# Optimization experiments

Measured on AMD Instinct MI355X. Metric: run time of the kernel, lower is better.

The kernel has to match this reference:

```python
import jax, jax.numpy as jnp
import numpy as np

N_NODES = 50000
N_EDGES = 800000
N_GRAPHS = 512
IN_CH = 7
HID = 128
FC = 128
N_CLASSES = 2
NEG_SLOPE = 0.2


def setup_inputs() -> dict:
    key = jax.random.key(0)
    ks = jax.random.split(key, 20)
    x = jax.random.normal(ks[0], (N_NODES, IN_CH), dtype=jnp.float32)
    edge_index = jax.random.randint(ks[1], (2, N_EDGES), 0, N_NODES, dtype=jnp.int64)
    batch = jnp.sort(jax.random.randint(ks[2], (N_NODES,), 0, N_GRAPHS, dtype=jnp.int64))
    inp = {"x": x, "edge_index": edge_index, "batch": batch}
    dims = [(IN_CH, HID), (HID, HID), (HID, HID)]
    for l, (din, dout) in enumerate(dims):
        inp[f"W{l}"] = jax.random.normal(ks[3 + 4 * l], (din, dout), dtype=jnp.float32) * (1.0 / np.sqrt(din))
        inp[f"a_src{l}"] = jax.random.normal(ks[4 + 4 * l], (dout,), dtype=jnp.float32) * 0.1
        inp[f"a_dst{l}"] = jax.random.normal(ks[5 + 4 * l], (dout,), dtype=jnp.float32) * 0.1
        inp[f"b{l}"] = jnp.zeros((dout,), dtype=jnp.float32)
    inp["fc1_w"] = jax.random.normal(ks[15], (HID, FC), dtype=jnp.float32) * (1.0 / np.sqrt(HID))
    inp["fc1_b"] = jnp.zeros((FC,), dtype=jnp.float32)
    inp["fc2_w"] = jax.random.normal(ks[16], (FC, N_CLASSES), dtype=jnp.float32) * (1.0 / np.sqrt(FC))
    inp["fc2_b"] = jnp.zeros((N_CLASSES,), dtype=jnp.float32)
    return inp


def _gat_conv(x, src, dst, W, a_s, a_d, b):
    # x: [N, din] -> h: [N, dout]
    h = x @ W
    alpha_src = h @ a_s  # [N]
    alpha_dst = h @ a_d  # [N]
    e = alpha_src[src] + alpha_dst[dst]  # [E]
    e = jnp.where(e > 0, e, NEG_SLOPE * e)  # LeakyReLU(0.2)
    # segment softmax over destination node neighborhoods
    m = jax.ops.segment_max(e, dst, num_segments=N_NODES)
    m = jnp.where(jnp.isfinite(m), m, 0.0)
    e = jnp.exp(e - m[dst])
    s = jax.ops.segment_sum(e, dst, num_segments=N_NODES)
    alpha = e / (s[dst] + 1e-16)  # [E]
    out = jax.ops.segment_sum(alpha[:, None] * h[src], dst, num_segments=N_NODES)
    return out + b


def _forward(x, edge_index, batch, params):
    # PyG GATConv default: add self-loops
    loop = jnp.arange(N_NODES, dtype=edge_index.dtype)
    src = jnp.concatenate([edge_index[0], loop])
    dst = jnp.concatenate([edge_index[1], loop])
    for l in range(3):
        W, a_s, a_d, b = params[f"W{l}"], params[f"a_src{l}"], params[f"a_dst{l}"], params[f"b{l}"]
        x = jax.nn.elu(_gat_conv(x, src, dst, W, a_s, a_d, b))
    # global mean pool over graphs
    sums = jax.ops.segment_sum(x, batch, num_segments=N_GRAPHS)  # [G, HID]
    cnt = jax.ops.segment_sum(jnp.ones((N_NODES,), x.dtype), batch, num_segments=N_GRAPHS)
    g = sums / jnp.maximum(cnt, 1.0)[:, None]
    h = jax.nn.relu(g @ params["fc1_w"] + params["fc1_b"])
    logits = h @ params["fc2_w"] + params["fc2_b"]
    return jax.nn.log_softmax(logits, axis=1)


def reference(x, edge_index, batch, W0, a_src0, a_dst0, b0, W1, a_src1, a_dst1, b1,
              W2, a_src2, a_dst2, b2, fc1_w, fc1_b, fc2_w, fc2_b):
    params = {"W0": W0, "a_src0": a_src0, "a_dst0": a_dst0, "b0": b0,
              "W1": W1, "a_src1": a_src1, "a_dst1": a_dst1, "b1": b1,
              "W2": W2, "a_src2": a_src2, "a_dst2": a_dst2, "b2": b2,
              "fc1_w": fc1_w, "fc1_b": fc1_b, "fc2_w": fc2_w, "fc2_b": fc2_b}
    return _forward(x, edge_index, batch, params)
```

## Files before the change

kernel.cpp:

```cpp
#include <hip/hip_runtime.h>
#include <math.h>

#define N_NODES 50000
#define N_EDGES 800000
#define N_GRAPHS 512
#define IN_CH 7
#define HID 128
#define FC 128
#define ET (N_EDGES + N_NODES)
#define NEG_SLOPE 0.2f


__global__ void k_init_deg(int* __restrict__ deg) {
  int i = blockIdx.x * blockDim.x + threadIdx.x;
  if (i < N_NODES) deg[i] = 1;
}

__global__ void k_hist(const int* __restrict__ dst, int* __restrict__ deg) {
  int i = blockIdx.x * blockDim.x + threadIdx.x;
  if (i < N_EDGES) atomicAdd(&deg[dst[i]], 1);
}

__global__ __launch_bounds__(1024) void k_scan(const int* __restrict__ deg,
                                               int* __restrict__ row_start,
                                               int* __restrict__ cursor) {
  __shared__ int wsum[16];
  __shared__ int s_carry;
  int tid = threadIdx.x;
  int lane = tid & 63, wid = tid >> 6;
  if (tid == 0) s_carry = 0;
  __syncthreads();
  for (int base = 0; base < N_NODES; base += 1024) {
    int i = base + tid;
    int v = (i < N_NODES) ? deg[i] : 0;
    int inc = v;
    #pragma unroll
    for (int off = 1; off < 64; off <<= 1) {
      int t = __shfl_up(inc, off, 64);
      if (lane >= off) inc += t;
    }
    if (lane == 63) wsum[wid] = inc;
    __syncthreads();
    if (wid == 0) {
      int wv = (lane < 16) ? wsum[lane] : 0;
      #pragma unroll
      for (int off = 1; off < 16; off <<= 1) {
        int t = __shfl_up(wv, off, 64);
        if (lane >= off) wv += t;
      }
      if (lane < 16) wsum[lane] = wv;
    }
    __syncthreads();
    int woff = (wid > 0) ? wsum[wid - 1] : 0;
    int incl = s_carry + woff + inc;
    int excl = incl - v;
    if (i < N_NODES) { row_start[i] = excl; cursor[i] = excl; }
    __syncthreads();
    if (tid == 1023) s_carry += wsum[15];
    __syncthreads();
  }
  if (tid == 0) row_start[N_NODES] = s_carry;
}

__global__ void k_fill(const int* __restrict__ esrc, const int* __restrict__ edst,
                       int* __restrict__ cursor, int* __restrict__ csr_src) {
  int i = blockIdx.x * blockDim.x + threadIdx.x;
  if (i < ET) {
    int s, d;
    if (i < N_EDGES) { s = esrc[i]; d = edst[i]; }
    else             { s = d = i - N_EDGES; }
    int pos = atomicAdd(&cursor[d], 1);
    csr_src[pos] = s;
  }
}


template<int DIN, int NPB>
__global__ __launch_bounds__(128) void k_gemm_small(const float* __restrict__ x,
                                                    const float* __restrict__ W,
                                                    const float* __restrict__ a_s,
                                                    const float* __restrict__ a_d,
                                                    float* __restrict__ h,
                                                    float* __restrict__ as_,
                                                    float* __restrict__ ad_) {
  __shared__ float Ws[DIN * HID];
  __shared__ float xs[DIN];
  __shared__ float red[4];
  int tid = threadIdx.x;
  for (int i = tid; i < DIN * HID; i += 128) Ws[i] = W[i];
  float asf = a_s[tid], adf = a_d[tid];
  int node0 = blockIdx.x * NPB;
  for (int nn = 0; nn < NPB; ++nn) {
    int node = node0 + nn;
    if (node >= N_NODES) break;
    __syncthreads();
    if (tid < DIN) xs[tid] = x[(size_t)node * DIN + tid];
    __syncthreads();
    float acc = 0.f;
    #pragma unroll
    for (int k = 0; k < DIN; ++k) acc = fmaf(xs[k], Ws[k * HID + tid], acc);
    h[(size_t)node * HID + tid] = acc;
    float vs = acc * asf, vd = acc * adf;
    #pragma unroll
    for (int off = 32; off >= 1; off >>= 1) {
      vs += __shfl_xor(vs, off, 64);
      vd += __shfl_xor(vd, off, 64);
    }
    int lane = tid & 63, wid = tid >> 6;
    if (lane == 0) { red[wid * 2] = vs; red[wid * 2 + 1] = vd; }
    __syncthreads();
    if (tid == 0)      as_[node] = red[0] + red[2];
    else if (tid == 1) ad_[node] = red[1] + red[3];
  }
}


#define GNPB 32

__global__ __launch_bounds__(128, 2) void k_gemm128(const float* __restrict__ x,
                                                    const float* __restrict__ W,
                                                    const float* __restrict__ a_s,
                                                    const float* __restrict__ a_d,
                                                    float* __restrict__ h,
                                                    float* __restrict__ as_,
                                                    float* __restrict__ ad_) {
  __shared__ float4 xs4[GNPB * 32];
  __shared__ float red[GNPB][4];
  int tid = threadIdx.x;
  int lane = tid & 63, wid = tid >> 6;

  float wreg[HID];
  #pragma unroll
  for (int k = 0; k < HID; ++k) wreg[k] = W[(size_t)k * HID + tid];
  float asf = a_s[tid], adf = a_d[tid];

  int node0 = blockIdx.x * GNPB;
  int rows = N_NODES - node0; if (rows > GNPB) rows = GNPB;

  const float4* xg = (const float4*)(x + (size_t)node0 * HID);
  for (int j = tid; j < rows * 32; j += 128) xs4[j] = xg[j];
  __syncthreads();

  for (int nn = 0; nn < rows; ++nn) {
    float acc = 0.f;
    #pragma unroll
    for (int k4 = 0; k4 < 32; ++k4) {
      float4 xv = xs4[nn * 32 + k4];
      acc = fmaf(xv.x, wreg[4 * k4 + 0], acc);
      acc = fmaf(xv.y, wreg[4 * k4 + 1], acc);
      acc = fmaf(xv.z, wreg[4 * k4 + 2], acc);
      acc = fmaf(xv.w, wreg[4 * k4 + 3], acc);
    }
    h[(size_t)(node0 + nn) * HID + tid] = acc;
    float vs = acc * asf, vd = acc * adf;
    #pragma unroll
    for (int off = 32; off >= 1; off >>= 1) {
      vs += __shfl_xor(vs, off, 64);
      vd += __shfl_xor(vd, off, 64);
    }
    if (lane == 0) { red[nn][wid * 2] = vs; red[nn][wid * 2 + 1] = vd; }
  }
  __syncthreads();
  if (tid < rows) {
    as_[node0 + tid] = red[tid][0] + red[tid][2];
  } else if (tid >= 64 && tid - 64 < rows) {
    int nn = tid - 64;
    ad_[node0 + nn] = red[nn][1] + red[nn][3];
  }
}


__global__ __launch_bounds__(256) void k_agg(const float* __restrict__ h,
                                             const float* __restrict__ as_,
                                             const float* __restrict__ ad_,
                                             const int* __restrict__ row_start,
                                             const int* __restrict__ csr_src,
                                             const float* __restrict__ b,
                                             float* __restrict__ out) {
  int wid = threadIdx.x >> 6, lane = threadIdx.x & 63;
  int node = blockIdx.x * 4 + wid;
  if (node >= N_NODES) return;
  int beg = row_start[node], end = row_start[node + 1];
  int n = end - beg;
  float adn = ad_[node];
  const float2* h2 = (const float2*)h;
  float a0 = 0.f, a1 = 0.f, c0 = 0.f, c1 = 0.f;
  float inv;

  if (n <= 64) {
    int sc_l = csr_src[beg + (lane < n ? lane : n - 1)];
    float e = as_[sc_l] + adn;
    e = e > 0.f ? e : NEG_SLOPE * e;
    float m = (lane < n) ? e : -INFINITY;
    #pragma unroll
    for (int off = 32; off >= 1; off >>= 1) m = fmaxf(m, __shfl_xor(m, off, 64));
    float we = (lane < n) ? __expf(e - m) : 0.f;
    float s = we;
    #pragma unroll
    for (int off = 32; off >= 1; off >>= 1) s += __shfl_xor(s, off, 64);
    inv = 1.f / (s + 1e-16f);
    int wbits = __float_as_int(we);

    int j = 0;
    for (; j + 4 <= n; j += 4) {
      int s0 = __builtin_amdgcn_readlane(sc_l, j);
      int s1 = __builtin_amdgcn_readlane(sc_l, j + 1);
      int s2 = __builtin_amdgcn_readlane(sc_l, j + 2);
      int s3 = __builtin_amdgcn_readlane(sc_l, j + 3);
      float w0 = __int_as_float(__builtin_amdgcn_readlane(wbits, j));
      float w1 = __int_as_float(__builtin_amdgcn_readlane(wbits, j + 1));
      float w2 = __int_as_float(__builtin_amdgcn_readlane(wbits, j + 2));
      float w3 = __int_as_float(__builtin_amdgcn_readlane(wbits, j + 3));
      float2 h0 = h2[(size_t)s0 * 64 + lane];
      float2 h1 = h2[(size_t)s1 * 64 + lane];
      float2 hh2 = h2[(size_t)s2 * 64 + lane];
      float2 h3 = h2[(size_t)s3 * 64 + lane];
      a0 = fmaf(w0, h0.x, a0);  a1 = fmaf(w0, h0.y, a1);
      c0 = fmaf(w1, h1.x, c0);  c1 = fmaf(w1, h1.y, c1);
      a0 = fmaf(w2, hh2.x, a0); a1 = fmaf(w2, hh2.y, a1);
      c0 = fmaf(w3, h3.x, c0);  c1 = fmaf(w3, h3.y, c1);
    }
    for (; j < n; ++j) {
      int sj = __builtin_amdgcn_readlane(sc_l, j);
      float wj = __int_as_float(__builtin_amdgcn_readlane(wbits, j));
      float2 hv = h2[(size_t)sj * 64 + lane];
      a0 = fmaf(wj, hv.x, a0);  a1 = fmaf(wj, hv.y, a1);
    }
  } else {
    float m = -INFINITY;
    for (int i = beg + lane; i < end; i += 64) {
      float e = as_[csr_src[i]] + adn;
      e = e > 0.f ? e : NEG_SLOPE * e;
      m = fmaxf(m, e);
    }
    #pragma unroll
    for (int off = 32; off >= 1; off >>= 1) m = fmaxf(m, __shfl_xor(m, off, 64));
    float s = 0.f;
    for (int i = beg; i < end; ++i) {
      int sc = csr_src[i];
      float e = as_[sc] + adn;
      e = e > 0.f ? e : NEG_SLOPE * e;
      float w = __expf(e - m);
      s += w;
      float2 hv = h2[(size_t)sc * 64 + lane];
      a0 = fmaf(w, hv.x, a0);
      a1 = fmaf(w, hv.y, a1);
    }
    inv = 1.f / (s + 1e-16f);
  }

  float2 bv = ((const float2*)b)[lane];
  float v0 = (a0 + c0) * inv + bv.x;
  float v1 = (a1 + c1) * inv + bv.y;
  v0 = v0 > 0.f ? v0 : expm1f(v0);
  v1 = v1 > 0.f ? v1 : expm1f(v1);
  float2 ov; ov.x = v0; ov.y = v1;
  ((float2*)out)[(size_t)node * 64 + lane] = ov;
}


__global__ __launch_bounds__(128) void k_pool_mlp(const float* __restrict__ x,
                                                  const int* __restrict__ batch,
                                                  const float* __restrict__ fc1_w,
                                                  const float* __restrict__ fc1_b,
                                                  const float* __restrict__ fc2_w,
                                                  const float* __restrict__ fc2_b,
                                                  float* __restrict__ out) {
  __shared__ float g[HID];
  __shared__ float h1[HID];
  __shared__ float lgs[2];
  int gid = blockIdx.x, tid = threadIdx.x;
  int a = 0, bnd = N_NODES;
  while (a < bnd) { int mid = (a + bnd) >> 1; if (batch[mid] < gid) a = mid + 1; else bnd = mid; }
  int lo = a;
  bnd = N_NODES;
  while (a < bnd) { int mid = (a + bnd) >> 1; if (batch[mid] < gid + 1) a = mid + 1; else bnd = mid; }
  int hi = a;
  float acc = 0.f;
  for (int n = lo; n < hi; ++n) acc += x[(size_t)n * HID + tid];
  float cnt = (float)(hi - lo);
  g[tid] = acc / fmaxf(cnt, 1.f);
  __syncthreads();
  float a1 = fc1_b[tid];
  #pragma unroll 8
  for (int k = 0; k < HID; ++k) a1 = fmaf(g[k], fc1_w[k * FC + tid], a1);
  a1 = fmaxf(a1, 0.f);
  h1[tid] = a1;
  __syncthreads();
  int lane = tid & 63, w = tid >> 6;
  float p = h1[lane] * fc2_w[lane * 2 + w] + h1[64 + lane] * fc2_w[(64 + lane) * 2 + w];
  #pragma unroll
  for (int off = 32; off >= 1; off >>= 1) p += __shfl_xor(p, off, 64);
  if (lane == 0) lgs[w] = p + fc2_b[w];
  __syncthreads();
  if (tid == 0) {
    float l0 = lgs[0], l1 = lgs[1];
    float mx = fmaxf(l0, l1);
    float lse = mx + logf(expf(l0 - mx) + expf(l1 - mx));
    out[gid * 2 + 0] = l0 - lse;
    out[gid * 2 + 1] = l1 - lse;
  }
}


extern "C" void kernel_launch(void* const* d_in, const int* in_sizes, int n_in,
                              void* d_out, int out_size, void* d_ws, size_t ws_size,
                              hipStream_t stream) {
  const float* x_in  = (const float*)d_in[0];
  const int*   eidx  = (const int*)d_in[1];
  const int*   batch = (const int*)d_in[2];
  const float* W0 = (const float*)d_in[3];
  const float* aS0 = (const float*)d_in[4];
  const float* aD0 = (const float*)d_in[5];
  const float* b0 = (const float*)d_in[6];
  const float* W1 = (const float*)d_in[7];
  const float* aS1 = (const float*)d_in[8];
  const float* aD1 = (const float*)d_in[9];
  const float* b1 = (const float*)d_in[10];
  const float* W2 = (const float*)d_in[11];
  const float* aS2 = (const float*)d_in[12];
  const float* aD2 = (const float*)d_in[13];
  const float* b2 = (const float*)d_in[14];
  const float* fc1_w = (const float*)d_in[15];
  const float* fc1_b = (const float*)d_in[16];
  const float* fc2_w = (const float*)d_in[17];
  const float* fc2_b = (const float*)d_in[18];
  float* out = (float*)d_out;

  char* ws = (char*)d_ws;
  float* h   = (float*)ws;  ws += (size_t)N_NODES * HID * sizeof(float);
  float* xb  = (float*)ws;  ws += (size_t)N_NODES * HID * sizeof(float);
  float* as_ = (float*)ws;  ws += (size_t)N_NODES * sizeof(float);
  float* ad_ = (float*)ws;  ws += (size_t)N_NODES * sizeof(float);
  int* row_start = (int*)ws; ws += (size_t)(N_NODES + 1) * sizeof(int);
  int* cursor    = (int*)ws; ws += (size_t)N_NODES * sizeof(int);
  int* deg       = (int*)ws; ws += (size_t)N_NODES * sizeof(int);
  int* csr_src   = (int*)ws; ws += (size_t)ET * sizeof(int);

  const int* esrc = eidx;
  const int* edst = eidx + N_EDGES;

  k_init_deg<<<(N_NODES + 255) / 256, 256, 0, stream>>>(deg);
  k_hist<<<(N_EDGES + 255) / 256, 256, 0, stream>>>(edst, deg);
  k_scan<<<1, 1024, 0, stream>>>(deg, row_start, cursor);
  k_fill<<<(ET + 255) / 256, 256, 0, stream>>>(esrc, edst, cursor, csr_src);

  int gemm_grid = (N_NODES + GNPB - 1) / GNPB;
  int agg_grid = (N_NODES + 3) / 4;

  k_gemm_small<IN_CH, 32><<<gemm_grid, 128, 0, stream>>>(x_in, W0, aS0, aD0, h, as_, ad_);
  k_agg<<<agg_grid, 256, 0, stream>>>(h, as_, ad_, row_start, csr_src, b0, xb);
  k_gemm128<<<gemm_grid, 128, 0, stream>>>(xb, W1, aS1, aD1, h, as_, ad_);
  k_agg<<<agg_grid, 256, 0, stream>>>(h, as_, ad_, row_start, csr_src, b1, xb);
  k_gemm128<<<gemm_grid, 128, 0, stream>>>(xb, W2, aS2, aD2, h, as_, ad_);
  k_agg<<<agg_grid, 256, 0, stream>>>(h, as_, ad_, row_start, csr_src, b2, xb);

  k_pool_mlp<<<N_GRAPHS, 128, 0, stream>>>(xb, batch, fc1_w, fc1_b, fc2_w, fc2_b, out);
}
```

Before: 622.8 us.

## Rewrite 128x128 GEMM as 64x64 register-tiled kernel with atomic attention dots

Replaces the per-thread-column GEMM, which held all of W in registers and computed one output per node per thread, with a shared-memory tiled kernel. Each 256-thread block computes a 64-node by 64-column tile, and each thread accumulates a 4x4 register block from a transposed x tile and a W tile. Because the output columns are now split across two blocks, the attention dot products are reduced within 16-lane groups and then added with atomics into as_/ad_. This requires an extra zeroing kernel before each GEMM and makes the summation order nondeterministic. The aim is more arithmetic per shared-memory load and less register pressure than the old 128-register W cache.

New measurement: 570.1 us. 8.5% less time.

```diff
diff --git a/kernel.cpp b/kernel.cpp
--- a/kernel.cpp
+++ b/kernel.cpp
@@ -72,6 +72,11 @@
     int pos = atomicAdd(&cursor[d], 1);
     csr_src[pos] = s;
   }
+}
+
+__global__ void k_zero(float* __restrict__ p, int n) {
+  int i = blockIdx.x * blockDim.x + threadIdx.x;
+  if (i < n) p[i] = 0.f;
 }
 
 
@@ -115,57 +120,97 @@
 }
 
 
-#define GNPB 32
-
-__global__ __launch_bounds__(128, 2) void k_gemm128(const float* __restrict__ x,
+#define TM 64
+#define TN 64
+
+__global__ __launch_bounds__(256, 2) void k_gemm128(const float* __restrict__ x,
                                                     const float* __restrict__ W,
                                                     const float* __restrict__ a_s,
                                                     const float* __restrict__ a_d,
                                                     float* __restrict__ h,
                                                     float* __restrict__ as_,
                                                     float* __restrict__ ad_) {
-  __shared__ float4 xs4[GNPB * 32];
-  __shared__ float red[GNPB][4];
+  __shared__ float xT[HID][TM + 4];
+  __shared__ float Wl[HID][TN + 4];
   int tid = threadIdx.x;
-  int lane = tid & 63, wid = tid >> 6;
-
-  float wreg[HID];
+  int node0 = blockIdx.x * TM;
+  int col0  = blockIdx.y * TN;
+
+  {
+    const float4* xg = (const float4*)x;
+    #pragma unroll
+    for (int it = 0; it < (TM * 32) / 256; ++it) {
+      int idx = tid + it * 256;
+      int r = idx >> 5, k4 = idx & 31;
+      int node = node0 + r;
+      float4 v = make_float4(0.f, 0.f, 0.f, 0.f);
+      if (node < N_NODES) v = xg[(size_t)node * 32 + k4];
+      xT[4 * k4 + 0][r] = v.x;
+      xT[4 * k4 + 1][r] = v.y;
+      xT[4 * k4 + 2][r] = v.z;
+      xT[4 * k4 + 3][r] = v.w;
+    }
+  }
+  {
+    const float4* wg = (const float4*)W;
+    #pragma unroll
+    for (int it = 0; it < (HID * (TN / 4)) / 256; ++it) {
+      int idx = tid + it * 256;
+      int k = idx >> 4, c4 = idx & 15;
+      float4 v = wg[(size_t)k * 32 + (col0 >> 2) + c4];
+      *(float4*)&Wl[k][4 * c4] = v;
+    }
+  }
+  __syncthreads();
+
+  int cg = tid & 15;
+  int nr = tid >> 4;
+  float acc00 = 0.f, acc01 = 0.f, acc02 = 0.f, acc03 = 0.f;
+  float acc10 = 0.f, acc11 = 0.f, acc12 = 0.f, acc13 = 0.f;
+  float acc20 = 0.f, acc21 = 0.f, acc22 = 0.f, acc23 = 0.f;
+  float acc30 = 0.f, acc31 = 0.f, acc32 = 0.f, acc33 = 0.f;
+
+  #pragma unroll 8
+  for (int k = 0; k < HID; ++k) {
+    float4 xv = *(const float4*)&xT[k][nr * 4];
+    float4 wv = *(const float4*)&Wl[k][cg * 4];
+    acc00 = fmaf(xv.x, wv.x, acc00); acc01 = fmaf(xv.x, wv.y, acc01);
+    acc02 = fmaf(xv.x, wv.z, acc02); acc03 = fmaf(xv.x, wv.w, acc03);
+    acc10 = fmaf(xv.y, wv.x, acc10); acc11 = fmaf(xv.y, wv.y, acc11);
+    acc12 = fmaf(xv.y, wv.z, acc12); acc13 = fmaf(xv.y, wv.w, acc13);
+    acc20 = fmaf(xv.z, wv.x, acc20); acc21 = fmaf(xv.z, wv.y, acc21);
+    acc22 = fmaf(xv.z, wv.z, acc22); acc23 = fmaf(xv.z, wv.w, acc23);
+    acc30 = fmaf(xv.w, wv.x, acc30); acc31 = fmaf(xv.w, wv.y, acc31);
+    acc32 = fmaf(xv.w, wv.z, acc32); acc33 = fmaf(xv.w, wv.w, acc33);
+  }
+
+  float as0 = a_s[col0 + 4 * cg + 0], as1 = a_s[col0 + 4 * cg + 1];
+  float as2 = a_s[col0 + 4 * cg + 2], as3 = a_s[col0 + 4 * cg + 3];
+  float ad0 = a_d[col0 + 4 * cg + 0], ad1 = a_d[col0 + 4 * cg + 1];
+  float ad2 = a_d[col0 + 4 * cg + 2], ad3 = a_d[col0 + 4 * cg + 3];
+
   #pragma unroll
-  for (int k = 0; k < HID; ++k) wreg[k] = W[(size_t)k * HID + tid];
-  float asf = a_s[tid], adf = a_d[tid];
-
-  int node0 = blockIdx.x * GNPB;
-  int rows = N_NODES - node0; if (rows > GNPB) rows = GNPB;
-
-  const float4* xg = (const float4*)(x + (size_t)node0 * HID);
-  for (int j = tid; j < rows * 32; j += 128) xs4[j] = xg[j];
-  __syncthreads();
-
-  for (int nn = 0; nn < rows; ++nn) {
-    float acc = 0.f;
-    #pragma unroll
-    for (int k4 = 0; k4 < 32; ++k4) {
-      float4 xv = xs4[nn * 32 + k4];
-      acc = fmaf(xv.x, wreg[4 * k4 + 0], acc);
-      acc = fmaf(xv.y, wreg[4 * k4 + 1], acc);
-      acc = fmaf(xv.z, wreg[4 * k4 + 2], acc);
-      acc = fmaf(xv.w, wreg[4 * k4 + 3], acc);
-    }
-    h[(size_t)(node0 + nn) * HID + tid] = acc;
-    float vs = acc * asf, vd = acc * adf;
-    #pragma unroll
-    for (int off = 32; off >= 1; off >>= 1) {
-      vs += __shfl_xor(vs, off, 64);
-      vd += __shfl_xor(vd, off, 64);
-    }
-    if (lane == 0) { red[nn][wid * 2] = vs; red[nn][wid * 2 + 1] = vd; }
-  }
-  __syncthreads();
-  if (tid < rows) {
-    as_[node0 + tid] = red[tid][0] + red[tid][2];
-  } else if (tid >= 64 && tid - 64 < rows) {
-    int nn = tid - 64;
-    ad_[node0 + nn] = red[nn][1] + red[nn][3];
+  for (int i = 0; i < 4; ++i) {
+    float r0 = (i == 0) ? acc00 : (i == 1) ? acc10 : (i == 2) ? acc20 : acc30;
+    float r1 = (i == 0) ? acc01 : (i == 1) ? acc11 : (i == 2) ? acc21 : acc31;
+    float r2 = (i == 0) ? acc02 : (i == 1) ? acc12 : (i == 2) ? acc22 : acc32;
+    float r3 = (i == 0) ? acc03 : (i == 1) ? acc13 : (i == 2) ? acc23 : acc33;
+    int node = node0 + nr * 4 + i;
+    float ps = fmaf(r0, as0, fmaf(r1, as1, fmaf(r2, as2, r3 * as3)));
+    float pd = fmaf(r0, ad0, fmaf(r1, ad1, fmaf(r2, ad2, r3 * ad3)));
+    #pragma unroll
+    for (int off = 1; off < 16; off <<= 1) {
+      ps += __shfl_xor(ps, off, 16);
+      pd += __shfl_xor(pd, off, 16);
+    }
+    if (node < N_NODES) {
+      float4 hv; hv.x = r0; hv.y = r1; hv.z = r2; hv.w = r3;
+      *(float4*)&h[(size_t)node * HID + col0 + 4 * cg] = hv;
+      if (cg == 0) {
+        atomicAdd(&as_[node], ps);
+        atomicAdd(&ad_[node], pd);
+      }
+    }
   }
 }
 
@@ -345,14 +390,17 @@
   k_scan<<<1, 1024, 0, stream>>>(deg, row_start, cursor);
   k_fill<<<(ET + 255) / 256, 256, 0, stream>>>(esrc, edst, cursor, csr_src);
 
-  int gemm_grid = (N_NODES + GNPB - 1) / GNPB;
+  dim3 ggrid((N_NODES + TM - 1) / TM, HID / TN);
   int agg_grid = (N_NODES + 3) / 4;
-
-  k_gemm_small<IN_CH, 32><<<gemm_grid, 128, 0, stream>>>(x_in, W0, aS0, aD0, h, as_, ad_);
+  int zgrid = (2 * N_NODES + 255) / 256;
+
+  k_gemm_small<IN_CH, 32><<<(N_NODES + 31) / 32, 128, 0, stream>>>(x_in, W0, aS0, aD0, h, as_, ad_);
   k_agg<<<agg_grid, 256, 0, stream>>>(h, as_, ad_, row_start, csr_src, b0, xb);
-  k_gemm128<<<gemm_grid, 128, 0, stream>>>(xb, W1, aS1, aD1, h, as_, ad_);
+  k_zero<<<zgrid, 256, 0, stream>>>(as_, 2 * N_NODES);
+  k_gemm128<<<ggrid, 256, 0, stream>>>(xb, W1, aS1, aD1, h, as_, ad_);
   k_agg<<<agg_grid, 256, 0, stream>>>(h, as_, ad_, row_start, csr_src, b1, xb);
-  k_gemm128<<<gemm_grid, 128, 0, stream>>>(xb, W2, aS2, aD2, h, as_, ad_);
+  k_zero<<<zgrid, 256, 0, stream>>>(as_, 2 * N_NODES);
+  k_gemm128<<<ggrid, 256, 0, stream>>>(xb, W2, aS2, aD2, h, as_, ad_);
   k_agg<<<agg_grid, 256, 0, stream>>>(h, as_, ad_, row_start, csr_src, b2, xb);
 
   k_pool_mlp<<<N_GRAPHS, 128, 0, stream>>>(xb, batch, fc1_w, fc1_b, fc2_w, fc2_b, out);
```
